# Kernel tuning notes

Hardware: AMD Instinct MI355X
Metric: run time of the kernel (lower is better)

## Reference

```python
import jax, jax.numpy as jnp
import numpy as np


def setup_inputs() -> dict:
    key = jax.random.key(0)
    ks = jax.random.split(key, 5)
    B, N, F, S = 8, 128, 32, 8
    F_ = 32          # output channels
    H = 32           # kernel_network hidden width
    node_features = jax.random.normal(ks[0], (B, N, F), dtype=jnp.float32)
    fltr = jax.random.uniform(ks[1], (B, N, N), dtype=jnp.float32)
    edge_features = jax.random.normal(ks[2], (B, N, N, S), dtype=jnp.float32)
    W0 = jax.random.normal(ks[3], (S, H), dtype=jnp.float32) * (1.0 / np.sqrt(S))
    b0 = jnp.zeros((H,), dtype=jnp.float32)
    W_out = jax.random.normal(ks[4], (H, F_ * F), dtype=jnp.float32) * (1.0 / np.sqrt(H))
    b_out = jnp.zeros((F_ * F,), dtype=jnp.float32)
    bias = jnp.zeros((F_,), dtype=jnp.float32)
    return {"node_features": node_features, "fltr": fltr, "edge_features": edge_features,
            "W0": W0, "b0": b0, "W_out": W_out, "b_out": b_out, "bias": bias}


def reference(node_features, fltr, edge_features, W0, b0, W_out, b_out, bias):
    B, N, F = node_features.shape
    F_ = bias.shape[0]
    # row-normalize the filter (adjacency)
    fltr_n = fltr / jnp.maximum(jnp.sum(fltr, axis=-1, keepdims=True), 1e-11)
    # kernel-generating network over edge features: (B,N,N,S) -> (B,N,N,F_*F)
    h = jax.nn.relu(edge_features @ W0 + b0)
    kernel = (h @ W_out + b_out).reshape(B, N, N, F_, F)
    # scale by normalized filter and aggregate neighbors:
    # out[a,b,c] = sum_{i,f} fltr_n[a,b,i] * kernel[a,b,i,c,f] * nf[a,i,f]
    out = jnp.einsum('abi,abicf,aif->abc', fltr_n, kernel, node_features)
    out = out + bias  # (B,N,F_)
    return out
```

## Files before the change

kernel.cpp:

```cpp
#include <hip/hip_runtime.h>

#define Bn 8
#define Nn 128
#define Fdim 32
#define Sdim 8
#define Hdim 32
#define Fout 32

__global__ __launch_bounds__(256, 4) void ecc_kernel(
    const float* __restrict__ nf,
    const float* __restrict__ fltr,
    const float* __restrict__ ef,
    const float* __restrict__ W0,
    const float* __restrict__ b0,
    const float* __restrict__ Wout,
    const float* __restrict__ bout,
    const float* __restrict__ bias,
    float* __restrict__ out)
{
    __shared__ __align__(16) float nf_s[Nn * Fdim];
    __shared__ __align__(16) float hbuf[Nn * Hdim];
    __shared__ __align__(16) float efTs[Nn * Sdim];
    __shared__ float fn_s[Nn];
    __shared__ __align__(16) float W0s[Sdim * Hdim];
    __shared__ float b0s[Hdim];
    __shared__ __align__(16) float qs[Fdim];
    __shared__ float inv_s;

    const int t   = threadIdx.x;
    const int blk = blockIdx.x;
    const int a   = blk >> 7;

    {
        const float4* nsrc = (const float4*)(nf + (size_t)a * Nn * Fdim);
        float4* ndst = (float4*)nf_s;
        #pragma unroll
        for (int j = 0; j < 4; ++j) ndst[j * 256 + t] = nsrc[j * 256 + t];
        ((float4*)efTs)[t] = ((const float4*)(ef + (size_t)blk * Nn * Sdim))[t];
    }
    if (t < Nn)          fn_s[t] = fltr[(size_t)blk * Nn + t];
    if (t < Sdim * Hdim) W0s[t]  = W0[t];
    if (t < Hdim)        b0s[t]  = b0[t];
    __syncthreads();

    if (t < 64) {
        float s = fn_s[t] + fn_s[t + 64];
        #pragma unroll
        for (int off = 32; off > 0; off >>= 1) s += __shfl_down(s, off);
        if (t == 0) inv_s = 1.0f / fmaxf(s, 1e-11f);
    }

    {
        const int hcol = t & 31, il = t >> 3 >> 2;
        #pragma unroll 4
        for (int k = 0; k < 16; ++k) {
            const int i = il * 16 + k;
            float acc = b0s[hcol];
            #pragma unroll
            for (int s = 0; s < Sdim; ++s)
                acc += efTs[i * Sdim + s] * W0s[s * Hdim + hcol];
            hbuf[i * Hdim + hcol] = fmaxf(acc, 0.0f) * fn_s[i];
        }
    }
    __syncthreads();

    {
        const int h = t & 31, fq = t >> 5;
        float4 accT = make_float4(0.f, 0.f, 0.f, 0.f);
        #pragma unroll 8
        for (int i = 0; i < Nn; ++i) {
            const float  hv = hbuf[i * Hdim + h];
            const float4 nv = *(const float4*)&nf_s[i * Fdim + fq * 4];
            accT.x += hv * nv.x; accT.y += hv * nv.y;
            accT.z += hv * nv.z; accT.w += hv * nv.w;
        }
        *(float4*)&efTs[h * Fdim + fq * 4] = accT;
    }
    if (t >= 224) {
        const int f = t - 224;
        float q = 0.f;
        #pragma unroll 4
        for (int i = 0; i < Nn; ++i) q += fn_s[i] * nf_s[i * Fdim + f];
        qs[f] = q;
    }
    __syncthreads();

    {
        const int c = t >> 3, f4 = t & 7;
        const float* wbase = Wout + (size_t)c * Fdim + f4 * 4;
        float partial = 0.f;
        #pragma unroll 4
        for (int h = 0; h < Hdim; ++h) {
            const float4 wv = *(const float4*)(wbase + (size_t)h * (Fout * Fdim));
            const float4 tv = *(const float4*)&efTs[h * Fdim + f4 * 4];
            partial += tv.x * wv.x + tv.y * wv.y + tv.z * wv.z + tv.w * wv.w;
        }
        {
            const float4 bv = *(const float4*)(bout + (size_t)c * Fdim + f4 * 4);
            const float4 qv = *(const float4*)&qs[f4 * 4];
            partial += qv.x * bv.x + qv.y * bv.y + qv.z * bv.z + qv.w * bv.w;
        }
        partial += __shfl_down(partial, 4, 8);
        partial += __shfl_down(partial, 2, 8);
        partial += __shfl_down(partial, 1, 8);
        if (f4 == 0)
            out[(size_t)blk * Fout + c] = partial * inv_s + bias[c];
    }
}

extern "C" void kernel_launch(void* const* d_in, const int* in_sizes, int n_in,
                              void* d_out, int out_size, void* d_ws, size_t ws_size,
                              hipStream_t stream) {
    const float* nf   = (const float*)d_in[0];
    const float* fltr = (const float*)d_in[1];
    const float* ef   = (const float*)d_in[2];
    const float* W0   = (const float*)d_in[3];
    const float* b0   = (const float*)d_in[4];
    const float* Wout = (const float*)d_in[5];
    const float* bout = (const float*)d_in[6];
    const float* bias = (const float*)d_in[7];
    float* out = (float*)d_out;

    ecc_kernel<<<dim3(Bn * Nn), dim3(256), 0, stream>>>(
        nf, fltr, ef, W0, b0, Wout, bout, bias, out);
}
```

Measured before the change: 83.53 us.

## Split neighbor reduction across thread halves and keep W0 in registers

Measured after the change: 80.74 us. 1.03x faster.

```diff
diff --git a/kernel.cpp b/kernel.cpp
--- a/kernel.cpp
+++ b/kernel.cpp
@@ -20,27 +20,29 @@
 {
     __shared__ __align__(16) float nf_s[Nn * Fdim];
     __shared__ __align__(16) float hbuf[Nn * Hdim];
-    __shared__ __align__(16) float efTs[Nn * Sdim];
+    __shared__ __align__(16) float efs[Nn * Sdim];
+    __shared__ __align__(16) float qp[Nn];
     __shared__ float fn_s[Nn];
-    __shared__ __align__(16) float W0s[Sdim * Hdim];
-    __shared__ float b0s[Hdim];
-    __shared__ __align__(16) float qs[Fdim];
     __shared__ float inv_s;
 
-    const int t   = threadIdx.x;
-    const int blk = blockIdx.x;
-    const int a   = blk >> 7;
+    const int t    = threadIdx.x;
+    const int blk  = blockIdx.x;
+    const int a    = blk >> 7;
+    const int hcol = t & 31;
+
+    float w0r[8];
+    #pragma unroll
+    for (int s = 0; s < Sdim; ++s) w0r[s] = W0[s * Hdim + hcol];
+    const float b0r = b0[hcol];
 
     {
         const float4* nsrc = (const float4*)(nf + (size_t)a * Nn * Fdim);
         float4* ndst = (float4*)nf_s;
         #pragma unroll
         for (int j = 0; j < 4; ++j) ndst[j * 256 + t] = nsrc[j * 256 + t];
-        ((float4*)efTs)[t] = ((const float4*)(ef + (size_t)blk * Nn * Sdim))[t];
+        ((float4*)efs)[t] = ((const float4*)(ef + (size_t)blk * Nn * Sdim))[t];
     }
-    if (t < Nn)          fn_s[t] = fltr[(size_t)blk * Nn + t];
-    if (t < Sdim * Hdim) W0s[t]  = W0[t];
-    if (t < Hdim)        b0s[t]  = b0[t];
+    if (t < Nn) fn_s[t] = fltr[(size_t)blk * Nn + t];
     __syncthreads();
 
     if (t < 64) {
@@ -51,37 +53,60 @@
     }
 
     {
-        const int hcol = t & 31, il = t >> 3 >> 2;
+        const int il = t >> 5;
         #pragma unroll 4
         for (int k = 0; k < 16; ++k) {
             const int i = il * 16 + k;
-            float acc = b0s[hcol];
-            #pragma unroll
-            for (int s = 0; s < Sdim; ++s)
-                acc += efTs[i * Sdim + s] * W0s[s * Hdim + hcol];
+            const float4 e0 = *(const float4*)&efs[i * Sdim];
+            const float4 e1 = *(const float4*)&efs[i * Sdim + 4];
+            float acc = b0r;
+            acc += e0.x * w0r[0] + e0.y * w0r[1] + e0.z * w0r[2] + e0.w * w0r[3];
+            acc += e1.x * w0r[4] + e1.y * w0r[5] + e1.z * w0r[6] + e1.w * w0r[7];
             hbuf[i * Hdim + hcol] = fmaxf(acc, 0.0f) * fn_s[i];
         }
     }
     __syncthreads();
 
+    const int fq   = t & 7;
+    const int h0   = ((t >> 3) & 15) * 2;
+    const int half = t >> 7;
+    float4 acc0 = make_float4(0.f, 0.f, 0.f, 0.f);
+    float4 acc1 = make_float4(0.f, 0.f, 0.f, 0.f);
     {
-        const int h = t & 31, fq = t >> 5;
-        float4 accT = make_float4(0.f, 0.f, 0.f, 0.f);
+        const int ibase = half * 64;
         #pragma unroll 8
-        for (int i = 0; i < Nn; ++i) {
-            const float  hv = hbuf[i * Hdim + h];
+        for (int k = 0; k < 64; ++k) {
+            const int i = ibase + k;
+            const float2 hv = *(const float2*)&hbuf[i * Hdim + h0];
             const float4 nv = *(const float4*)&nf_s[i * Fdim + fq * 4];
-            accT.x += hv * nv.x; accT.y += hv * nv.y;
-            accT.z += hv * nv.z; accT.w += hv * nv.w;
+            acc0.x += hv.x * nv.x; acc0.y += hv.x * nv.y;
+            acc0.z += hv.x * nv.z; acc0.w += hv.x * nv.w;
+            acc1.x += hv.y * nv.x; acc1.y += hv.y * nv.y;
+            acc1.z += hv.y * nv.z; acc1.w += hv.y * nv.w;
         }
-        *(float4*)&efTs[h * Fdim + fq * 4] = accT;
     }
-    if (t >= 224) {
-        const int f = t - 224;
+    if (half) {
+        float4* p = (float4*)&efs[(t - 128) * 8];
+        p[0] = acc0; p[1] = acc1;
+    }
+    __syncthreads();
+
+    if (!half) {
+        const float4* p = (const float4*)&efs[t * 8];
+        const float4 p0 = p[0], p1 = p[1];
+        acc0.x += p0.x; acc0.y += p0.y; acc0.z += p0.z; acc0.w += p0.w;
+        acc1.x += p1.x; acc1.y += p1.y; acc1.z += p1.z; acc1.w += p1.w;
+        *(float4*)&hbuf[h0 * Fdim + fq * 4]       = acc0;
+        *(float4*)&hbuf[(h0 + 1) * Fdim + fq * 4] = acc1;
+    } else {
+        const int f = t & 31, qr = (t >> 5) & 3;
         float q = 0.f;
         #pragma unroll 4
-        for (int i = 0; i < Nn; ++i) q += fn_s[i] * nf_s[i * Fdim + f];
-        qs[f] = q;
+        for (int k = 0; k < 32; ++k) {
+            const int i = qr * 32 + k;
+            q += fn_s[i] * nf_s[i * Fdim + f];
+        }
+        qp[qr * 32 + f] = q;
     }
     __syncthreads();
 
@@ -89,16 +114,22 @@
         const int c = t >> 3, f4 = t & 7;
         const float* wbase = Wout + (size_t)c * Fdim + f4 * 4;
         float partial = 0.f;
-        #pragma unroll 4
+        #pragma unroll 8
         for (int h = 0; h < Hdim; ++h) {
             const float4 wv = *(const float4*)(wbase + (size_t)h * (Fout * Fdim));
-            const float4 tv = *(const float4*)&efTs[h * Fdim + f4 * 4];
+            const float4 tv = *(const float4*)&hbuf[h * Fdim + f4 * 4];
             partial += tv.x * wv.x + tv.y * wv.y + tv.z * wv.z + tv.w * wv.w;
         }
         {
+            const float4 q0 = *(const float4*)&qp[f4 * 4];
+            const float4 q1 = *(const float4*)&qp[32 + f4 * 4];
+            const float4 q2 = *(const float4*)&qp[64 + f4 * 4];
+            const float4 q3 = *(const float4*)&qp[96 + f4 * 4];
             const float4 bv = *(const float4*)(bout + (size_t)c * Fdim + f4 * 4);
-            const float4 qv = *(const float4*)&qs[f4 * 4];
-            partial += qv.x * bv.x + qv.y * bv.y + qv.z * bv.z + qv.w * bv.w;
+            partial += (q0.x + q1.x + q2.x + q3.x) * bv.x;
+            partial += (q0.y + q1.y + q2.y + q3.y) * bv.y;
+            partial += (q0.z + q1.z + q2.z + q3.z) * bv.z;
+            partial += (q0.w + q1.w + q2.w + q3.w) * bv.w;
         }
         partial += __shfl_down(partial, 4, 8);
         partial += __shfl_down(partial, 2, 8);
```
